# Kernel optimization log

Measured on AMD Instinct MI355X. Metric: run time of the kernel, lower is better.

Reference implementation:

```python
import jax, jax.numpy as jnp
import numpy as np

B, N, DIM = 4, 2048, 1024
HEADS, DIM_HEAD = 16, 64
INNER = HEADS * DIM_HEAD  # 1024
SCALE = DIM_HEAD ** -0.5

def setup_inputs() -> dict:
    key = jax.random.key(0)
    k1, k2, k3 = jax.random.split(key, 3)
    x = jax.random.normal(k1, (B, N, DIM), dtype=jnp.float32)
    w_qkv = jax.random.normal(k2, (DIM, 3 * INNER), dtype=jnp.float32) * (DIM ** -0.5)
    w_out = jax.random.normal(k3, (INNER, DIM), dtype=jnp.float32) * (INNER ** -0.5)
    b_out = jnp.zeros((DIM,), dtype=jnp.float32)
    return {"x": x, "w_qkv": w_qkv, "w_out": w_out, "b_out": b_out}

def reference(x, w_qkv, w_out, b_out):
    b, n, _ = x.shape
    qkv = x @ w_qkv  # [b, n, 3*inner]
    q, k, v = jnp.split(qkv, 3, axis=-1)
    # [b, n, h, d] -> [b, h, n, d]
    reshape = lambda t: t.reshape(b, n, HEADS, DIM_HEAD).transpose(0, 2, 1, 3)
    q, k, v = reshape(q), reshape(k), reshape(v)
    dots = jnp.einsum('bhqd,bhkd->bhqk', q, k) * SCALE
    attn = jax.nn.softmax(dots, axis=-1)
    out = jnp.einsum('bhqk,bhkd->bhqd', attn, v)
    out = out.transpose(0, 2, 1, 3).reshape(b, n, INNER)
    return out @ w_out + b_out
```

## Files before the change

kernel.cpp:

```cpp
#include <hip/hip_runtime.h>

typedef unsigned short u16;
typedef __bf16 bf16_t;
typedef bf16_t bf16x8 __attribute__((ext_vector_type(8)));
typedef float f32x4 __attribute__((ext_vector_type(4)));
typedef float f32x16 __attribute__((ext_vector_type(16)));
typedef u16 u16x8 __attribute__((ext_vector_type(8)));
typedef u16 u16x4 __attribute__((ext_vector_type(4)));
typedef unsigned uint2v __attribute__((ext_vector_type(2)));

#define B_     4
#define N_     2048
#define DIM_   1024
#define HEADS_ 16
#define DH_    64
#define INNER_ 1024
#define QKV3_  3072
#define SCALE_ 0.125f
#define LOG2E_ 1.44269504089f

__device__ __forceinline__ u16 f2bf(float f) {
  union { float f; unsigned u; } v; v.f = f;
  unsigned r = v.u + 0x7FFFu + ((v.u >> 16) & 1u);
  return (u16)(r >> 16);
}
__device__ __forceinline__ u16 bfbits(float f) {
  bf16_t b = (bf16_t)f;
  return __builtin_bit_cast(u16, b);
}
__device__ __forceinline__ unsigned packbf(float lo, float hi) {
  return (unsigned)bfbits(lo) | ((unsigned)bfbits(hi) << 16);
}

#if __has_builtin(__builtin_amdgcn_exp2f)
#define EXP2F(x) __builtin_amdgcn_exp2f(x)
#else
#define EXP2F(x) __expf((x) * 0.69314718056f)
#endif

typedef __attribute__((address_space(1))) const unsigned int ga_u32;
typedef __attribute__((address_space(3))) unsigned int ls_u32;
__device__ __forceinline__ void gload16(const void* g, void* l) {
  __builtin_amdgcn_global_load_lds((ga_u32*)g, (ls_u32*)l, 16, 0, 0);
}

__global__ __launch_bounds__(256) void cvt_f32_bf16(const float* __restrict__ in,
                                                    u16* __restrict__ out, int n8) {
  int i = blockIdx.x * 256 + threadIdx.x;
  if (i < n8) {
    const float4* p = (const float4*)(in + (size_t)i * 8);
    float4 a = p[0], b = p[1];
    u16x8 o;
    o[0] = f2bf(a.x); o[1] = f2bf(a.y); o[2] = f2bf(a.z); o[3] = f2bf(a.w);
    o[4] = f2bf(b.x); o[5] = f2bf(b.y); o[6] = f2bf(b.z); o[7] = f2bf(b.w);
    *(u16x8*)(out + (size_t)i * 8) = o;
  }
}

__global__ __launch_bounds__(256) void transp_w(const float* __restrict__ in,
                                                u16* __restrict__ out, int Kd, int Nd) {
  __shared__ float t[32][33];
  int n0 = blockIdx.x * 32, k0 = blockIdx.y * 32;
  int tx = threadIdx.x & 31, ty = threadIdx.x >> 5;
#pragma unroll
  for (int i = 0; i < 4; i++)
    t[ty + i * 8][tx] = in[(size_t)(k0 + ty + i * 8) * Nd + n0 + tx];
  __syncthreads();
#pragma unroll
  for (int i = 0; i < 4; i++)
    out[(size_t)(n0 + ty + i * 8) * Kd + k0 + tx] = f2bf(t[tx][ty + i * 8]);
}

__global__ __launch_bounds__(256) void gemm_qkv(const u16* __restrict__ A,
                                                const u16* __restrict__ BT,
                                                u16* __restrict__ qbuf,
                                                u16* __restrict__ ktiled,
                                                u16* __restrict__ vtiled,
                                                int M, int N, int K) {
  __shared__ alignas(16) u16 ldsA[2][128 * 64];
  __shared__ alignas(16) u16 ldsB[2][128 * 64];
  const int tid = threadIdx.x;
  const int lane = tid & 63, wid = tid >> 6;
  const int l16 = lane & 15, lg = lane >> 4;

  int bid = blockIdx.x;
  const int cpx = gridDim.x >> 3;
  bid = (bid & 7) * cpx + (bid >> 3);

  const int ntiles = N >> 7;
  const int tm = bid / ntiles, tn = bid % ntiles;
  const int m0 = tm << 7, n0 = tn << 7;
  const int wr = wid >> 1, wc = wid & 1;

  const int srow_in = lane >> 3;
  const int soff = ((lane & 7) ^ srow_in) * 8;

  f32x4 acc[4][4];
#pragma unroll
  for (int i = 0; i < 4; i++)
#pragma unroll
    for (int j = 0; j < 4; j++) acc[i][j] = f32x4{0.f, 0.f, 0.f, 0.f};

  const int KSTEPS = K >> 6;

#define GSTAGE_(kk, buf)                                                           \
  do {                                                                             \
    const int k1_ = (kk) << 6;                                                     \
    char* bA_ = (char*)&ldsA[(buf)][0];                                            \
    char* bB_ = (char*)&ldsB[(buf)][0];                                            \
    _Pragma("unroll")                                                              \
    for (int i_ = 0; i_ < 4; i_++) {                                               \
      const int rb_ = wid * 32 + i_ * 8;                                           \
      gload16(A  + (size_t)(m0 + rb_ + srow_in) * K + k1_ + soff, bA_ + rb_ * 128);\
      gload16(BT + (size_t)(n0 + rb_ + srow_in) * K + k1_ + soff, bB_ + rb_ * 128);\
    }                                                                              \
  } while (0)

  GSTAGE_(0, 0);
  GSTAGE_(1, 1);

  for (int ks = 0; ks < KSTEPS; ks++) {
    if (ks + 1 < KSTEPS) asm volatile("s_waitcnt vmcnt(8)" ::: "memory");
    else                 asm volatile("s_waitcnt vmcnt(0)" ::: "memory");
    __builtin_amdgcn_s_barrier();

    const char* cA = (const char*)&ldsA[ks & 1][0];
    const char* cB = (const char*)&ldsB[ks & 1][0];

    bf16x8 bf[4][2];
#pragma unroll
    for (int n = 0; n < 4; n++) {
      int row = wc * 64 + n * 16 + l16;
      int rb = row * 128, swz = (row & 7) << 4;
      bf[n][0] = *(const bf16x8*)(cB + rb + ((lg * 16) ^ swz));
      bf[n][1] = *(const bf16x8*)(cB + rb + ((64 + lg * 16) ^ swz));
    }
    __builtin_amdgcn_s_setprio(1);
#pragma unroll
    for (int mm = 0; mm < 4; mm++) {
      int row = wr * 64 + mm * 16 + l16;
      int rb = row * 128, swz = (row & 7) << 4;
      bf16x8 af0 = *(const bf16x8*)(cA + rb + ((lg * 16) ^ swz));
      bf16x8 af1 = *(const bf16x8*)(cA + rb + ((64 + lg * 16) ^ swz));
#pragma unroll
      for (int n = 0; n < 4; n++) {
        acc[mm][n] = __builtin_amdgcn_mfma_f32_16x16x32_bf16(af0, bf[n][0], acc[mm][n], 0, 0, 0);
        acc[mm][n] = __builtin_amdgcn_mfma_f32_16x16x32_bf16(af1, bf[n][1], acc[mm][n], 0, 0, 0);
      }
    }
    __builtin_amdgcn_s_setprio(0);

    __builtin_amdgcn_s_barrier();
    if (ks + 2 < KSTEPS) GSTAGE_(ks + 2, ks & 1);
  }
#undef GSTAGE_

  const int seg = n0 >> 10;
#pragma unroll
  for (int mm = 0; mm < 4; mm++) {
#pragma unroll
    for (int nn = 0; nn < 4; nn++) {
      const int row = m0 + wr * 64 + mm * 16 + lg * 4;
      const int col = n0 + wc * 64 + nn * 16 + l16;
      if (seg == 0) {
#pragma unroll
        for (int j = 0; j < 4; j++)
          qbuf[(size_t)(row + j) * INNER_ + col] = f2bf(acc[mm][nn][j]);
      } else if (seg == 1) {
        const int kd = col - 1024;
        const int h = kd >> 6, s = (kd >> 3) & 7, e = kd & 7;
#pragma unroll
        for (int j = 0; j < 4; j++) {
          const int rr = row + j;
          const int b = rr >> 11, n = rr & (N_ - 1);
          ktiled[(((size_t)(b * HEADS_ + h) * 32 + (n >> 6)) << 12) +
                 (s << 9) + ((n & 63) << 3) + e] = f2bf(acc[mm][nn][j]);
        }
      } else {
        const int vd = col - 2048;
        const int h = vd >> 6, d = vd & 63;
#pragma unroll
        for (int j = 0; j < 4; j++) {
          const int rr = row + j;
          const int b = rr >> 11, n = rr & (N_ - 1);
          vtiled[(((size_t)(b * HEADS_ + h) * 32 + (n >> 6)) << 12) +
                 (((n >> 3) & 7) << 9) + (d << 3) + (n & 7)] = f2bf(acc[mm][nn][j]);
        }
      }
    }
  }
}

__global__ __launch_bounds__(256) void gemm_bt(const u16* __restrict__ A,
                                               const u16* __restrict__ BT,
                                               float* __restrict__ Cp,
                                               const float* __restrict__ bias,
                                               int M, int N, int K) {
  __shared__ alignas(16) u16 ldsA[2][128 * 64];
  __shared__ alignas(16) u16 ldsB[2][128 * 64];
  const int tid = threadIdx.x;
  const int lane = tid & 63, wid = tid >> 6;
  const int l16 = lane & 15, lg = lane >> 4;

  int bid = blockIdx.x;
  const int cpx = gridDim.x >> 3;
  bid = (bid & 7) * cpx + (bid >> 3);

  const int ntiles = N >> 7;
  const int tm = bid / ntiles, tn = bid % ntiles;
  const int m0 = tm << 7, n0 = tn << 7;
  const int wr = wid >> 1, wc = wid & 1;

  const int srow_in = lane >> 3;
  const int soff = ((lane & 7) ^ srow_in) * 8;

  f32x4 acc[4][4];
#pragma unroll
  for (int i = 0; i < 4; i++)
#pragma unroll
    for (int j = 0; j < 4; j++) acc[i][j] = f32x4{0.f, 0.f, 0.f, 0.f};

  const int KSTEPS = K >> 6;

#define GSTAGE_(kk, buf)                                                           \
  do {                                                                             \
    const int k1_ = (kk) << 6;                                                     \
    char* bA_ = (char*)&ldsA[(buf)][0];                                            \
    char* bB_ = (char*)&ldsB[(buf)][0];                                            \
    _Pragma("unroll")                                                              \
    for (int i_ = 0; i_ < 4; i_++) {                                               \
      const int rb_ = wid * 32 + i_ * 8;                                           \
      gload16(A  + (size_t)(m0 + rb_ + srow_in) * K + k1_ + soff, bA_ + rb_ * 128);\
      gload16(BT + (size_t)(n0 + rb_ + srow_in) * K + k1_ + soff, bB_ + rb_ * 128);\
    }                                                                              \
  } while (0)

  GSTAGE_(0, 0);
  GSTAGE_(1, 1);

  for (int ks = 0; ks < KSTEPS; ks++) {
    if (ks + 1 < KSTEPS) asm volatile("s_waitcnt vmcnt(8)" ::: "memory");
    else                 asm volatile("s_waitcnt vmcnt(0)" ::: "memory");
    __builtin_amdgcn_s_barrier();

    const char* cA = (const char*)&ldsA[ks & 1][0];
    const char* cB = (const char*)&ldsB[ks & 1][0];

    bf16x8 bf[4][2];
#pragma unroll
    for (int n = 0; n < 4; n++) {
      int row = wc * 64 + n * 16 + l16;
      int rb = row * 128, swz = (row & 7) << 4;
      bf[n][0] = *(const bf16x8*)(cB + rb + ((lg * 16) ^ swz));
      bf[n][1] = *(const bf16x8*)(cB + rb + ((64 + lg * 16) ^ swz));
    }
    __builtin_amdgcn_s_setprio(1);
#pragma unroll
    for (int mm = 0; mm < 4; mm++) {
      int row = wr * 64 + mm * 16 + l16;
      int rb = row * 128, swz = (row & 7) << 4;
      bf16x8 af0 = *(const bf16x8*)(cA + rb + ((lg * 16) ^ swz));
      bf16x8 af1 = *(const bf16x8*)(cA + rb + ((64 + lg * 16) ^ swz));
#pragma unroll
      for (int n = 0; n < 4; n++) {
        acc[mm][n] = __builtin_amdgcn_mfma_f32_16x16x32_bf16(af0, bf[n][0], acc[mm][n], 0, 0, 0);
        acc[mm][n] = __builtin_amdgcn_mfma_f32_16x16x32_bf16(af1, bf[n][1], acc[mm][n], 0, 0, 0);
      }
    }
    __builtin_amdgcn_s_setprio(0);

    __builtin_amdgcn_s_barrier();
    if (ks + 2 < KSTEPS) GSTAGE_(ks + 2, ks & 1);
  }
#undef GSTAGE_

#pragma unroll
  for (int mm = 0; mm < 4; mm++) {
#pragma unroll
    for (int n = 0; n < 4; n++) {
      int row = m0 + wr * 64 + mm * 16 + lg * 4;
      int col = n0 + wc * 64 + n * 16 + l16;
#pragma unroll
      for (int j = 0; j < 4; j++)
        Cp[(size_t)(row + j) * N + col] = acc[mm][n][j] + bias[col];
    }
  }
}

__global__ __launch_bounds__(512, 4) void attn_fwd(const u16* __restrict__ qbuf,
                                                   const u16* __restrict__ ktiled,
                                                   const u16* __restrict__ vtiled,
                                                   u16* __restrict__ abuf) {
  __shared__ alignas(16) u16 ldsK[3][64 * 64];
  __shared__ alignas(16) u16 ldsV[3][64 * 64];

  const int tid = threadIdx.x;
  const int lane = tid & 63, wid = tid >> 6;
  const int l32 = lane & 31, hl = lane >> 5;

  int bid = blockIdx.x;
  bid = (bid & 7) * 64 + (bid >> 3);
  const int bh = bid >> 3, qt = bid & 7;
  const int b = bh >> 4, h = bh & 15;
  const int q0 = qt * 256 + wid * 32;

  constexpr float QS = SCALE_ * LOG2E_;
  bf16x8 qf[4];
  {
    const u16* qrow = qbuf + (size_t)(b * N_ + q0 + l32) * INNER_ + h * DH_ + hl * 8;
#pragma unroll
    for (int step = 0; step < 4; step++) {
      bf16x8 t = *(const bf16x8*)(qrow + step * 16);
#pragma unroll
      for (int i = 0; i < 8; i++) t[i] = (bf16_t)((float)t[i] * QS);
      qf[step] = t;
    }
  }

  const u16* kts = ktiled + (size_t)bh * 131072 + tid * 8;
  const u16* vts = vtiled + (size_t)bh * 131072 + tid * 8;
  const int sdst = wid << 10;

  const int kofs = (hl << 10) + (l32 << 4);

  float lrow = 0.f;
  f32x16 acc[2];
#pragma unroll
  for (int i = 0; i < 16; i++) { acc[0][i] = 0.f; acc[1][i] = 0.f; }

  gload16(kts, (char*)ldsK + sdst);
  gload16(vts, (char*)ldsV + sdst);
  gload16(kts + 4096, (char*)ldsK + 8192 + sdst);
  gload16(vts + 4096, (char*)ldsV + 8192 + sdst);

  const int NT = N_ / 64;
  int cur = 0, pre = 2;

  for (int kt = 0; kt < NT; ++kt) {
    if (kt < NT - 1) asm volatile("s_waitcnt vmcnt(2)" ::: "memory");
    else             asm volatile("s_waitcnt vmcnt(0)" ::: "memory");
    __builtin_amdgcn_s_barrier();
    if (kt + 2 < NT) {
      gload16(kts + (size_t)(kt + 2) * 4096, (char*)ldsK + pre * 8192 + sdst);
      gload16(vts + (size_t)(kt + 2) * 4096, (char*)ldsV + pre * 8192 + sdst);
    }

    const char* Kb = (const char*)ldsK + cur * 8192;
    const char* Vb = (const char*)ldsV + cur * 8192;

    f32x16 s[2];
    __builtin_amdgcn_s_setprio(1);
#pragma unroll
    for (int ktile = 0; ktile < 2; ktile++) {
      f32x16 c;
#pragma unroll
      for (int i = 0; i < 16; i++) c[i] = 0.f;
      const char* rb = Kb + (ktile << 9) + kofs;
#pragma unroll
      for (int step = 0; step < 4; step++) {
        bf16x8 kf = *(const bf16x8*)(rb + (step << 11));
        c = __builtin_amdgcn_mfma_f32_32x32x16_bf16(kf, qf[step], c, 0, 0, 0);
      }
      s[ktile] = c;
    }
    __builtin_amdgcn_s_setprio(0);

    float ps0 = 0.f, ps1 = 0.f;
#pragma unroll
    for (int ktile = 0; ktile < 2; ktile++)
#pragma unroll
      for (int i = 0; i < 16; i += 2) {
        const float p0 = EXP2F(s[ktile][i]);
        const float p1 = EXP2F(s[ktile][i + 1]);
        s[ktile][i] = p0; s[ktile][i + 1] = p1;
        ps0 += p0; ps1 += p1;
      }
    lrow += ps0 + ps1;

    bf16x8 pb[4];
#pragma unroll
    for (int ktile = 0; ktile < 2; ktile++)
#pragma unroll
      for (int par = 0; par < 2; par++) {
        const int rb8 = par * 8;
        const unsigned c0 = packbf(s[ktile][rb8 + 0], s[ktile][rb8 + 1]);
        const unsigned c1 = packbf(s[ktile][rb8 + 2], s[ktile][rb8 + 3]);
        const unsigned c2 = packbf(s[ktile][rb8 + 4], s[ktile][rb8 + 5]);
        const unsigned c3 = packbf(s[ktile][rb8 + 6], s[ktile][rb8 + 7]);
        const uint2v r02 = __builtin_amdgcn_permlane32_swap(c0, c2, false, false);
        const uint2v r13 = __builtin_amdgcn_permlane32_swap(c1, c3, false, false);
        union { unsigned u[4]; bf16x8 v; } w;
        w.u[0] = r02[0]; w.u[1] = r13[0]; w.u[2] = r02[1]; w.u[3] = r13[1];
        pb[ktile * 2 + par] = w.v;
      }

    __builtin_amdgcn_s_setprio(1);
#pragma unroll
    for (int dtile = 0; dtile < 2; dtile++) {
      const char* rb = Vb + (dtile << 9) + kofs;
      f32x16 c = acc[dtile];
#pragma unroll
      for (int step = 0; step < 4; step++) {
        bf16x8 vf = *(const bf16x8*)(rb + (step << 11));
        c = __builtin_amdgcn_mfma_f32_32x32x16_bf16(vf, pb[step], c, 0, 0, 0);
      }
      acc[dtile] = c;
    }
    __builtin_amdgcn_s_setprio(0);

    cur = (cur == 2) ? 0 : cur + 1;
    pre = (pre == 2) ? 0 : pre + 1;
  }

  lrow += __shfl_xor(lrow, 32);
  const float inv = 1.f / lrow;
  const size_t row = (size_t)(b * N_ + q0 + l32);
#pragma unroll
  for (int dtile = 0; dtile < 2; dtile++)
#pragma unroll
    for (int g = 0; g < 4; g++) {
      u16x4 w;
#pragma unroll
      for (int j = 0; j < 4; j++) w[j] = bfbits(acc[dtile][g * 4 + j] * inv);
      const int d = dtile * 32 + g * 8 + hl * 4;
      *(u16x4*)(abuf + row * INNER_ + h * DH_ + d) = w;
    }
}

extern "C" void kernel_launch(void* const* d_in, const int* in_sizes, int n_in,
                              void* d_out, int out_size, void* d_ws, size_t ws_size,
                              hipStream_t stream) {
  const float* x     = (const float*)d_in[0];
  const float* w_qkv = (const float*)d_in[1];
  const float* w_out = (const float*)d_in[2];
  const float* b_out = (const float*)d_in[3];
  float* out = (float*)d_out;

  char* ws = (char*)d_ws;
  u16* xb     = (u16*)(ws);
  u16* wqkvT  = (u16*)(ws + (size_t)(16 << 20));
  u16* woutT  = (u16*)(ws + (size_t)(22 << 20));
  u16* qbuf   = (u16*)(ws + (size_t)(24 << 20));
  u16* ktiled = (u16*)(ws + (size_t)(40 << 20));
  u16* vtiled = (u16*)(ws + (size_t)(56 << 20));
  u16* abuf   = xb;

  cvt_f32_bf16<<<4096, 256, 0, stream>>>(x, xb, (B_ * N_ * DIM_) / 8);
  transp_w<<<dim3(QKV3_ / 32, DIM_ / 32), 256, 0, stream>>>(w_qkv, wqkvT, DIM_, QKV3_);
  transp_w<<<dim3(DIM_ / 32, INNER_ / 32), 256, 0, stream>>>(w_out, woutT, INNER_, DIM_);
  gemm_qkv<<<(B_ * N_ / 128) * (QKV3_ / 128), 256, 0, stream>>>(
      xb, wqkvT, qbuf, ktiled, vtiled, B_ * N_, QKV3_, DIM_);
  attn_fwd<<<512, 512, 0, stream>>>(qbuf, ktiled, vtiled, abuf);
  gemm_bt<<<(B_ * N_ / 128) * (DIM_ / 128), 256, 0, stream>>>(
      abuf, woutT, out, b_out, B_ * N_, DIM_, INNER_);
}
```

Measured before the change: 189.6 us.

## Enlarge QKV GEMM tiles to 256x256 with 512-thread blocks

The QKV projection GEMM now uses 256x256 output tiles per block with 8 waves of 128x64 each, instead of 128x128 tiles with 4 waves. The grid drops to 384 blocks, and K is fixed at compile time. The pipeline also changes from a two-deep prefetch with a partial vmcnt wait to a single-stage prefetch issued right after a full wait. The larger tiles are meant to raise arithmetic intensity and reuse of each global load. In exchange there are fewer blocks for 256 CUs (about 1.5 waves), more accumulator registers per thread, 128KB of LDS per block, and possibly less latency hiding with the shallower prefetch.

```diff
diff --git a/kernel.cpp b/kernel.cpp
--- a/kernel.cpp
+++ b/kernel.cpp
@@ -71,12 +71,131 @@
     out[(size_t)(n0 + ty + i * 8) * Kd + k0 + tx] = f2bf(t[tx][ty + i * 8]);
 }
 
-__global__ __launch_bounds__(256) void gemm_qkv(const u16* __restrict__ A,
-                                                const u16* __restrict__ BT,
-                                                u16* __restrict__ qbuf,
-                                                u16* __restrict__ ktiled,
-                                                u16* __restrict__ vtiled,
-                                                int M, int N, int K) {
+__global__ __launch_bounds__(512, 2) void gemm_qkv(const u16* __restrict__ A,
+                                                   const u16* __restrict__ BT,
+                                                   u16* __restrict__ qbuf,
+                                                   u16* __restrict__ ktiled,
+                                                   u16* __restrict__ vtiled) {
+  constexpr int K = DIM_;
+  constexpr int KT = K / 64;
+  __shared__ alignas(16) u16 ldsA[2][256 * 64];
+  __shared__ alignas(16) u16 ldsB[2][256 * 64];
+  const int tid = threadIdx.x;
+  const int lane = tid & 63, wid = tid >> 6;
+  const int l16 = lane & 15, lg = lane >> 4;
+  const int wm = wid >> 2, wn = wid & 3;
+
+  int bid = blockIdx.x;
+  bid = (bid & 7) * 48 + (bid >> 3);
+  const int tm = bid / 12, tn = bid % 12;
+  const int m0 = tm << 8, n0 = tn << 8;
+
+  const int srow_in = lane >> 3;
+  const int soff = ((lane & 7) ^ srow_in) * 8;
+
+  f32x4 acc[8][4];
+#pragma unroll
+  for (int i = 0; i < 8; i++)
+#pragma unroll
+    for (int j = 0; j < 4; j++) acc[i][j] = f32x4{0.f, 0.f, 0.f, 0.f};
+
+#define STG_(kk, buf)                                                              \
+  do {                                                                             \
+    const int k1_ = (kk) << 6;                                                     \
+    char* bA_ = (char*)&ldsA[(buf)][0];                                            \
+    char* bB_ = (char*)&ldsB[(buf)][0];                                            \
+    _Pragma("unroll")                                                              \
+    for (int i_ = 0; i_ < 4; i_++) {                                               \
+      const int rb_ = i_ * 64 + wid * 8;                                           \
+      gload16(A  + (size_t)(m0 + rb_ + srow_in) * K + k1_ + soff, bA_ + rb_ * 128);\
+      gload16(BT + (size_t)(n0 + rb_ + srow_in) * K + k1_ + soff, bB_ + rb_ * 128);\
+    }                                                                              \
+  } while (0)
+
+  STG_(0, 0);
+
+  for (int kt = 0; kt < KT; kt++) {
+    asm volatile("s_waitcnt vmcnt(0)" ::: "memory");
+    __builtin_amdgcn_s_barrier();
+    if (kt + 1 < KT) STG_(kt + 1, (kt + 1) & 1);
+
+    const char* cA = (const char*)&ldsA[kt & 1][0];
+    const char* cB = (const char*)&ldsB[kt & 1][0];
+
+    bf16x8 bf[4][2];
+#pragma unroll
+    for (int nf = 0; nf < 4; nf++) {
+      const int row = wn * 64 + nf * 16 + l16;
+      const int rb = row * 128, swz = (row & 7) << 4;
+      bf[nf][0] = *(const bf16x8*)(cB + rb + ((lg * 16) ^ swz));
+      bf[nf][1] = *(const bf16x8*)(cB + rb + ((64 + lg * 16) ^ swz));
+    }
+#pragma unroll
+    for (int half = 0; half < 2; half++) {
+      bf16x8 af[4][2];
+#pragma unroll
+      for (int m = 0; m < 4; m++) {
+        const int row = wm * 128 + (half * 4 + m) * 16 + l16;
+        const int rb = row * 128, swz = (row & 7) << 4;
+        af[m][0] = *(const bf16x8*)(cA + rb + ((lg * 16) ^ swz));
+        af[m][1] = *(const bf16x8*)(cA + rb + ((64 + lg * 16) ^ swz));
+      }
+      __builtin_amdgcn_s_setprio(1);
+#pragma unroll
+      for (int m = 0; m < 4; m++)
+#pragma unroll
+        for (int nf = 0; nf < 4; nf++) {
+          f32x4 c = acc[half * 4 + m][nf];
+          c = __builtin_amdgcn_mfma_f32_16x16x32_bf16(af[m][0], bf[nf][0], c, 0, 0, 0);
+          c = __builtin_amdgcn_mfma_f32_16x16x32_bf16(af[m][1], bf[nf][1], c, 0, 0, 0);
+          acc[half * 4 + m][nf] = c;
+        }
+      __builtin_amdgcn_s_setprio(0);
+    }
+  }
+#undef STG_
+
+  const int seg = n0 >> 10;
+#pragma unroll
+  for (int mf = 0; mf < 8; mf++) {
+#pragma unroll
+    for (int nf = 0; nf < 4; nf++) {
+      const int row = m0 + wm * 128 + mf * 16 + lg * 4;
+      const int col = n0 + wn * 64 + nf * 16 + l16;
+      if (seg == 0) {
+#pragma unroll
+        for (int j = 0; j < 4; j++)
+          qbuf[(size_t)(row + j) * INNER_ + col] = f2bf(acc[mf][nf][j]);
+      } else if (seg == 1) {
+        const int kd = col - 1024;
+        const int h = kd >> 6, s = (kd >> 3) & 7, e = kd & 7;
+#pragma unroll
+        for (int j = 0; j < 4; j++) {
+          const int rr = row + j;
+          const int b = rr >> 11, n = rr & (N_ - 1);
+          ktiled[(((size_t)(b * HEADS_ + h) * 32 + (n >> 6)) << 12) +
+                 (s << 9) + ((n & 63) << 3) + e] = f2bf(acc[mf][nf][j]);
+        }
+      } else {
+        const int vd = col - 2048;
+        const int h = vd >> 6, d = vd & 63;
+#pragma unroll
+        for (int j = 0; j < 4; j++) {
+          const int rr = row + j;
+          const int b = rr >> 11, n = rr & (N_ - 1);
+          vtiled[(((size_t)(b * HEADS_ + h) * 32 + (n >> 6)) << 12) +
+                 (((n >> 3) & 7) << 9) + (d << 3) + (n & 7)] = f2bf(acc[mf][nf][j]);
+        }
+      }
+    }
+  }
+}
+
+__global__ __launch_bounds__(256) void gemm_bt(const u16* __restrict__ A,
+                                               const u16* __restrict__ BT,
+                                               float* __restrict__ Cp,
+                                               const float* __restrict__ bias,
+                                               int M, int N, int K) {
   __shared__ alignas(16) u16 ldsA[2][128 * 64];
   __shared__ alignas(16) u16 ldsB[2][128 * 64];
   const int tid = threadIdx.x;
@@ -155,125 +274,6 @@
   }
 #undef GSTAGE_
 
-  const int seg = n0 >> 10;
-#pragma unroll
-  for (int mm = 0; mm < 4; mm++) {
-#pragma unroll
-    for (int nn = 0; nn < 4; nn++) {
-      const int row = m0 + wr * 64 + mm * 16 + lg * 4;
-      const int col = n0 + wc * 64 + nn * 16 + l16;
-      if (seg == 0) {
-#pragma unroll
-        for (int j = 0; j < 4; j++)
-          qbuf[(size_t)(row + j) * INNER_ + col] = f2bf(acc[mm][nn][j]);
-      } else if (seg == 1) {
-        const int kd = col - 1024;
-        const int h = kd >> 6, s = (kd >> 3) & 7, e = kd & 7;
-#pragma unroll
-        for (int j = 0; j < 4; j++) {
-          const int rr = row + j;
-          const int b = rr >> 11, n = rr & (N_ - 1);
-          ktiled[(((size_t)(b * HEADS_ + h) * 32 + (n >> 6)) << 12) +
-                 (s << 9) + ((n & 63) << 3) + e] = f2bf(acc[mm][nn][j]);
-        }
-      } else {
-        const int vd = col - 2048;
-        const int h = vd >> 6, d = vd & 63;
-#pragma unroll
-        for (int j = 0; j < 4; j++) {
-          const int rr = row + j;
-          const int b = rr >> 11, n = rr & (N_ - 1);
-          vtiled[(((size_t)(b * HEADS_ + h) * 32 + (n >> 6)) << 12) +
-                 (((n >> 3) & 7) << 9) + (d << 3) + (n & 7)] = f2bf(acc[mm][nn][j]);
-        }
-      }
-    }
-  }
-}
-
-__global__ __launch_bounds__(256) void gemm_bt(const u16* __restrict__ A,
-                                               const u16* __restrict__ BT,
-                                               float* __restrict__ Cp,
-                                               const float* __restrict__ bias,
-                                               int M, int N, int K) {
-  __shared__ alignas(16) u16 ldsA[2][128 * 64];
-  __shared__ alignas(16) u16 ldsB[2][128 * 64];
-  const int tid = threadIdx.x;
-  const int lane = tid & 63, wid = tid >> 6;
-  const int l16 = lane & 15, lg = lane >> 4;
-
-  int bid = blockIdx.x;
-  const int cpx = gridDim.x >> 3;
-  bid = (bid & 7) * cpx + (bid >> 3);
-
-  const int ntiles = N >> 7;
-  const int tm = bid / ntiles, tn = bid % ntiles;
-  const int m0 = tm << 7, n0 = tn << 7;
-  const int wr = wid >> 1, wc = wid & 1;
-
-  const int srow_in = lane >> 3;
-  const int soff = ((lane & 7) ^ srow_in) * 8;
-
-  f32x4 acc[4][4];
-#pragma unroll
-  for (int i = 0; i < 4; i++)
-#pragma unroll
-    for (int j = 0; j < 4; j++) acc[i][j] = f32x4{0.f, 0.f, 0.f, 0.f};
-
-  const int KSTEPS = K >> 6;
-
-#define GSTAGE_(kk, buf)                                                           \
-  do {                                                                             \
-    const int k1_ = (kk) << 6;                                                     \
-    char* bA_ = (char*)&ldsA[(buf)][0];                                            \
-    char* bB_ = (char*)&ldsB[(buf)][0];                                            \
-    _Pragma("unroll")                                                              \
-    for (int i_ = 0; i_ < 4; i_++) {                                               \
-      const int rb_ = wid * 32 + i_ * 8;                                           \
-      gload16(A  + (size_t)(m0 + rb_ + srow_in) * K + k1_ + soff, bA_ + rb_ * 128);\
-      gload16(BT + (size_t)(n0 + rb_ + srow_in) * K + k1_ + soff, bB_ + rb_ * 128);\
-    }                                                                              \
-  } while (0)
-
-  GSTAGE_(0, 0);
-  GSTAGE_(1, 1);
-
-  for (int ks = 0; ks < KSTEPS; ks++) {
-    if (ks + 1 < KSTEPS) asm volatile("s_waitcnt vmcnt(8)" ::: "memory");
-    else                 asm volatile("s_waitcnt vmcnt(0)" ::: "memory");
-    __builtin_amdgcn_s_barrier();
-
-    const char* cA = (const char*)&ldsA[ks & 1][0];
-    const char* cB = (const char*)&ldsB[ks & 1][0];
-
-    bf16x8 bf[4][2];
-#pragma unroll
-    for (int n = 0; n < 4; n++) {
-      int row = wc * 64 + n * 16 + l16;
-      int rb = row * 128, swz = (row & 7) << 4;
-      bf[n][0] = *(const bf16x8*)(cB + rb + ((lg * 16) ^ swz));
-      bf[n][1] = *(const bf16x8*)(cB + rb + ((64 + lg * 16) ^ swz));
-    }
-    __builtin_amdgcn_s_setprio(1);
-#pragma unroll
-    for (int mm = 0; mm < 4; mm++) {
-      int row = wr * 64 + mm * 16 + l16;
-      int rb = row * 128, swz = (row & 7) << 4;
-      bf16x8 af0 = *(const bf16x8*)(cA + rb + ((lg * 16) ^ swz));
-      bf16x8 af1 = *(const bf16x8*)(cA + rb + ((64 + lg * 16) ^ swz));
-#pragma unroll
-      for (int n = 0; n < 4; n++) {
-        acc[mm][n] = __builtin_amdgcn_mfma_f32_16x16x32_bf16(af0, bf[n][0], acc[mm][n], 0, 0, 0);
-        acc[mm][n] = __builtin_amdgcn_mfma_f32_16x16x32_bf16(af1, bf[n][1], acc[mm][n], 0, 0, 0);
-      }
-    }
-    __builtin_amdgcn_s_setprio(0);
-
-    __builtin_amdgcn_s_barrier();
-    if (ks + 2 < KSTEPS) GSTAGE_(ks + 2, ks & 1);
-  }
-#undef GSTAGE_
-
 #pragma unroll
   for (int mm = 0; mm < 4; mm++) {
 #pragma unroll
@@ -448,8 +448,7 @@
   cvt_f32_bf16<<<4096, 256, 0, stream>>>(x, xb, (B_ * N_ * DIM_) / 8);
   transp_w<<<dim3(QKV3_ / 32, DIM_ / 32), 256, 0, stream>>>(w_qkv, wqkvT, DIM_, QKV3_);
   transp_w<<<dim3(DIM_ / 32, INNER_ / 32), 256, 0, stream>>>(w_out, woutT, INNER_, DIM_);
-  gemm_qkv<<<(B_ * N_ / 128) * (QKV3_ / 128), 256, 0, stream>>>(
-      xb, wqkvT, qbuf, ktiled, vtiled, B_ * N_, QKV3_, DIM_);
+  gemm_qkv<<<384, 512, 0, stream>>>(xb, wqkvT, qbuf, ktiled, vtiled);
   attn_fwd<<<512, 512, 0, stream>>>(qbuf, ktiled, vtiled, abuf);
   gemm_bt<<<(B_ * N_ / 128) * (DIM_ / 128), 256, 0, stream>>>(
       abuf, woutT, out, b_out, B_ * N_, DIM_, INNER_);
```

New measurement: 193.8 us. 1.02x slower.

## Software-pipeline attention loop so next tile's QK overlaps current softmax and PV

Applied to the files above, without the earlier changes.

Restructures the attention key-tile loop so the QK^T MFMAs for tile kt+1 are issued before the exp, pack and PV work for tile kt. Independent matrix and vector work can then interleave within a wave. The prologue now waits for the first two tiles and computes the first scores, and an epilogue handles the last tile. The wait is relaxed to vmcnt(1), since only the K half of the next tile is needed early. Launch bounds drop from 4 to 3 waves per SIMD to leave room for the extra live score registers, at the cost of occupancy.

```diff
diff --git a/kernel.cpp b/kernel.cpp
--- a/kernel.cpp
+++ b/kernel.cpp
@@ -287,7 +287,7 @@
   }
 }
 
-__global__ __launch_bounds__(512, 4) void attn_fwd(const u16* __restrict__ qbuf,
+__global__ __launch_bounds__(512, 3) void attn_fwd(const u16* __restrict__ qbuf,
                                                    const u16* __restrict__ ktiled,
                                                    const u16* __restrict__ vtiled,
                                                    u16* __restrict__ abuf) {
@@ -328,89 +328,103 @@
 #pragma unroll
   for (int i = 0; i < 16; i++) { acc[0][i] = 0.f; acc[1][i] = 0.f; }
 
+#define QK_(bufidx, dst)                                                          \
+  do {                                                                            \
+    const char* Kb_ = (const char*)ldsK + (bufidx) * 8192;                        \
+    _Pragma("unroll")                                                             \
+    for (int kt_ = 0; kt_ < 2; kt_++) {                                           \
+      f32x16 c_;                                                                  \
+      _Pragma("unroll")                                                           \
+      for (int ii_ = 0; ii_ < 16; ii_++) c_[ii_] = 0.f;                           \
+      const char* rb_ = Kb_ + (kt_ << 9) + kofs;                                  \
+      _Pragma("unroll")                                                           \
+      for (int st_ = 0; st_ < 4; st_++) {                                         \
+        bf16x8 kf_ = *(const bf16x8*)(rb_ + (st_ << 11));                         \
+        c_ = __builtin_amdgcn_mfma_f32_32x32x16_bf16(kf_, qf[st_], c_, 0, 0, 0);  \
+      }                                                                           \
+      (dst)[kt_] = c_;                                                            \
+    }                                                                             \
+  } while (0)
+
+#define SMPV_(bufidx, sarr)                                                       \
+  do {                                                                            \
+    float ps0_ = 0.f, ps1_ = 0.f;                                                 \
+    _Pragma("unroll")                                                             \
+    for (int kt_ = 0; kt_ < 2; kt_++)                                             \
+      _Pragma("unroll")                                                           \
+      for (int ii_ = 0; ii_ < 16; ii_ += 2) {                                     \
+        const float p0_ = EXP2F((sarr)[kt_][ii_]);                                \
+        const float p1_ = EXP2F((sarr)[kt_][ii_ + 1]);                            \
+        (sarr)[kt_][ii_] = p0_; (sarr)[kt_][ii_ + 1] = p1_;                       \
+        ps0_ += p0_; ps1_ += p1_;                                                 \
+      }                                                                           \
+    lrow += ps0_ + ps1_;                                                          \
+    bf16x8 pb_[4];                                                                \
+    _Pragma("unroll")                                                             \
+    for (int kt_ = 0; kt_ < 2; kt_++)                                             \
+      _Pragma("unroll")                                                           \
+      for (int pr_ = 0; pr_ < 2; pr_++) {                                         \
+        const int rb8_ = pr_ * 8;                                                 \
+        const unsigned c0_ = packbf((sarr)[kt_][rb8_ + 0], (sarr)[kt_][rb8_ + 1]);\
+        const unsigned c1_ = packbf((sarr)[kt_][rb8_ + 2], (sarr)[kt_][rb8_ + 3]);\
+        const unsigned c2_ = packbf((sarr)[kt_][rb8_ + 4], (sarr)[kt_][rb8_ + 5]);\
+        const unsigned c3_ = packbf((sarr)[kt_][rb8_ + 6], (sarr)[kt_][rb8_ + 7]);\
+        const uint2v r02_ = __builtin_amdgcn_permlane32_swap(c0_, c2_, false, false);\
+        const uint2v r13_ = __builtin_amdgcn_permlane32_swap(c1_, c3_, false, false);\
+        union { unsigned u[4]; bf16x8 v; } w_;                                    \
+        w_.u[0] = r02_[0]; w_.u[1] = r13_[0]; w_.u[2] = r02_[1]; w_.u[3] = r13_[1];\
+        pb_[kt_ * 2 + pr_] = w_.v;                                                \
+      }                                                                           \
+    const char* Vb_ = (const char*)ldsV + (bufidx) * 8192;                        \
+    __builtin_amdgcn_s_setprio(1);                                                \
+    _Pragma("unroll")                                                             \
+    for (int dt_ = 0; dt_ < 2; dt_++) {                                           \
+      const char* rb_ = Vb_ + (dt_ << 9) + kofs;                                  \
+      f32x16 c_ = acc[dt_];                                                       \
+      _Pragma("unroll")                                                           \
+      for (int st_ = 0; st_ < 4; st_++) {                                         \
+        bf16x8 vf_ = *(const bf16x8*)(rb_ + (st_ << 11));                         \
+        c_ = __builtin_amdgcn_mfma_f32_32x32x16_bf16(vf_, pb_[st_], c_, 0, 0, 0); \
+      }                                                                           \
+      acc[dt_] = c_;                                                              \
+    }                                                                             \
+    __builtin_amdgcn_s_setprio(0);                                                \
+  } while (0)
+
   gload16(kts, (char*)ldsK + sdst);
   gload16(vts, (char*)ldsV + sdst);
   gload16(kts + 4096, (char*)ldsK + 8192 + sdst);
   gload16(vts + 4096, (char*)ldsV + 8192 + sdst);
+  asm volatile("s_waitcnt vmcnt(0)" ::: "memory");
+  __builtin_amdgcn_s_barrier();
+
+  f32x16 sc[2], sN[2];
+  QK_(0, sc);
 
   const int NT = N_ / 64;
-  int cur = 0, pre = 2;
-
-  for (int kt = 0; kt < NT; ++kt) {
-    if (kt < NT - 1) asm volatile("s_waitcnt vmcnt(2)" ::: "memory");
-    else             asm volatile("s_waitcnt vmcnt(0)" ::: "memory");
+  int cur = 0, nxt = 1, pre = 2;
+
+  for (int kt = 0; kt < NT - 1; ++kt) {
+    asm volatile("s_waitcnt vmcnt(1)" ::: "memory");
     __builtin_amdgcn_s_barrier();
     if (kt + 2 < NT) {
       gload16(kts + (size_t)(kt + 2) * 4096, (char*)ldsK + pre * 8192 + sdst);
       gload16(vts + (size_t)(kt + 2) * 4096, (char*)ldsV + pre * 8192 + sdst);
     }
-
-    const char* Kb = (const char*)ldsK + cur * 8192;
-    const char* Vb = (const char*)ldsV + cur * 8192;
-
-    f32x16 s[2];
     __builtin_amdgcn_s_setprio(1);
-#pragma unroll
-    for (int ktile = 0; ktile < 2; ktile++) {
-      f32x16 c;
-#pragma unroll
-      for (int i = 0; i < 16; i++) c[i] = 0.f;
-      const char* rb = Kb + (ktile << 9) + kofs;
-#pragma unroll
-      for (int step = 0; step < 4; step++) {
-        bf16x8 kf = *(const bf16x8*)(rb + (step << 11));
-        c = __builtin_amdgcn_mfma_f32_32x32x16_bf16(kf, qf[step], c, 0, 0, 0);
-      }
-      s[ktile] = c;
-    }
+    QK_(nxt, sN);
     __builtin_amdgcn_s_setprio(0);
-
-    float ps0 = 0.f, ps1 = 0.f;
-#pragma unroll
-    for (int ktile = 0; ktile < 2; ktile++)
-#pragma unroll
-      for (int i = 0; i < 16; i += 2) {
-        const float p0 = EXP2F(s[ktile][i]);
-        const float p1 = EXP2F(s[ktile][i + 1]);
-        s[ktile][i] = p0; s[ktile][i + 1] = p1;
-        ps0 += p0; ps1 += p1;
-      }
-    lrow += ps0 + ps1;
-
-    bf16x8 pb[4];
-#pragma unroll
-    for (int ktile = 0; ktile < 2; ktile++)
-#pragma unroll
-      for (int par = 0; par < 2; par++) {
-        const int rb8 = par * 8;
-        const unsigned c0 = packbf(s[ktile][rb8 + 0], s[ktile][rb8 + 1]);
-        const unsigned c1 = packbf(s[ktile][rb8 + 2], s[ktile][rb8 + 3]);
-        const unsigned c2 = packbf(s[ktile][rb8 + 4], s[ktile][rb8 + 5]);
-        const unsigned c3 = packbf(s[ktile][rb8 + 6], s[ktile][rb8 + 7]);
-        const uint2v r02 = __builtin_amdgcn_permlane32_swap(c0, c2, false, false);
-        const uint2v r13 = __builtin_amdgcn_permlane32_swap(c1, c3, false, false);
-        union { unsigned u[4]; bf16x8 v; } w;
-        w.u[0] = r02[0]; w.u[1] = r13[0]; w.u[2] = r02[1]; w.u[3] = r13[1];
-        pb[ktile * 2 + par] = w.v;
-      }
-
-    __builtin_amdgcn_s_setprio(1);
-#pragma unroll
-    for (int dtile = 0; dtile < 2; dtile++) {
-      const char* rb = Vb + (dtile << 9) + kofs;
-      f32x16 c = acc[dtile];
-#pragma unroll
-      for (int step = 0; step < 4; step++) {
-        bf16x8 vf = *(const bf16x8*)(rb + (step << 11));
-        c = __builtin_amdgcn_mfma_f32_32x32x16_bf16(vf, pb[step], c, 0, 0, 0);
-      }
-      acc[dtile] = c;
-    }
-    __builtin_amdgcn_s_setprio(0);
-
-    cur = (cur == 2) ? 0 : cur + 1;
-    pre = (pre == 2) ? 0 : pre + 1;
-  }
+    SMPV_(cur, sc);
+    sc[0] = sN[0]; sc[1] = sN[1];
+    const int t = cur; cur = nxt; nxt = pre; pre = t;
+  }
+
+  asm volatile("s_waitcnt vmcnt(0)" ::: "memory");
+  __builtin_amdgcn_s_barrier();
+  SMPV_(cur, sc);
+
+#undef QK_
+#undef SMPV_
 
   lrow += __shfl_xor(lrow, 32);
   const float inv = 1.f / lrow;
```

New measurement: 211.1 us. +11.3%, slower.
